# Kernel tuning notes

Measured on AMD Instinct MI355X. Metric: run time of the kernel, lower is better.

The kernel has to match this reference:

```python
import jax, jax.numpy as jnp
import numpy as np


def setup_inputs() -> dict:
    key = jax.random.key(0)
    ks = jax.random.split(key, 6)
    B, S, D = 32, 4096, 512
    return {
        "inputs": jax.random.normal(ks[0], (B, S, D), dtype=jnp.float32),
        "W_y": jax.random.normal(ks[1], (D, D), dtype=jnp.float32) * 0.05,
        "W_h": jax.random.normal(ks[2], (D, D), dtype=jnp.float32) * 0.05,
        "W_p": jax.random.normal(ks[3], (D, D), dtype=jnp.float32) * 0.05,
        "W_x": jax.random.normal(ks[4], (D, D), dtype=jnp.float32) * 0.05,
        "w": jax.random.normal(ks[5], (D, 1), dtype=jnp.float32) * 0.05,
    }


def reference(inputs, W_y, W_h, W_p, W_x, w):
    # inputs: [B, S, D]; the TF einsums 'ijk,kk->ijk' etc. use only diag(W).
    half = inputs.shape[1] // 2
    y = inputs[:, :half, :]          # [B, S/2, D] premise states
    h_n = inputs[:, -1, :]           # [B, D] final hidden state
    first = y * jnp.diagonal(W_y)                     # [B, S/2, D]
    second = (h_n * jnp.diagonal(W_h))[:, None, :]    # [B, 1, D] (RepeatVector via broadcast)
    M = jnp.tanh(first + second)                      # [B, S/2, D]
    scores = jnp.einsum('bsd,d->bs', M, w[:, 0])      # [B, S/2]
    alpha = jax.nn.softmax(scores, axis=-1)           # softmax over attended positions
    r = jnp.einsum('bsd,bs->bd', y, alpha)            # [B, D] weighted sum
    return jnp.tanh(r * jnp.diagonal(W_p) + h_n * jnp.diagonal(W_x))
```

## Files before the change

kernel.cpp:

```cpp
#include <hip/hip_runtime.h>

#define DDIM 512
#define HALF 2048
#define BATCH 32
#define S_TOTAL 4096
#define NCHUNK 64
#define ROWS_PER_CHUNK 32
#define LOG2E 1.44269504088896340736f
#define SHIFT2 32.0f

__device__ __forceinline__ float fast_tanh(float x) {
    float e = __builtin_amdgcn_exp2f(x * 2.88539008177792681472f);
    return 1.0f - 2.0f * __builtin_amdgcn_rcpf(e + 1.0f);
}

__device__ __forceinline__ float tanh_poly(float x) {
    const float c3 = -0.33333333333f, c5 = 0.13333333333f,
                c7 = -0.05396825397f, c9 = 0.02186948854f;
    float x2 = x * x;
    float p = fmaf(x2, c9, c7);
    p = fmaf(x2, p, c5);
    p = fmaf(x2, p, c3);
    return fmaf(x * x2, p, x);
}

template <int CTRL>
__device__ __forceinline__ float dpp_add(float x) {
    int yi = __builtin_amdgcn_update_dpp(0, __float_as_int(x), CTRL, 0xf, 0xf, true);
    return x + __int_as_float(yi);
}

__device__ __forceinline__ float wave_reduce_sum(float p) {
    p = dpp_add<0xB1>(p);
    p = dpp_add<0x4E>(p);
    p = dpp_add<0x141>(p);
    p = dpp_add<0x140>(p);
    p += __int_as_float(__builtin_amdgcn_ds_swizzle(__float_as_int(p), 0x401F));
    p += __shfl_xor(p, 32);
    return p;
}

__global__ __launch_bounds__(256) void pass1_kernel(
    const float* __restrict__ inputs, const float* __restrict__ Wy,
    const float* __restrict__ Wh, const float* __restrict__ wvec,
    float* __restrict__ ws_l, float* __restrict__ ws_r)
{
    const int chunk = blockIdx.x;
    const int b = blockIdx.y;
    const int tid = threadIdx.x;
    const int wave = tid >> 6;
    const int lane = tid & 63;
    const int d0 = lane * 8;

    float wy[8], wv[8], c[8];
    {
        const float* hn_row = inputs + ((size_t)b * S_TOTAL + (S_TOTAL - 1)) * DDIM;
#pragma unroll
        for (int j = 0; j < 8; ++j) {
            const int d = d0 + j;
            wy[j] = Wy[(size_t)d * (DDIM + 1)];
            wv[j] = wvec[d];
            c[j]  = hn_row[d] * Wh[(size_t)d * (DDIM + 1)];
        }
    }

    const float* rb0 = inputs +
        ((size_t)b * S_TOTAL + (size_t)chunk * ROWS_PER_CHUNK + wave * 8) * DDIM + d0;
    float y[8][8];
#pragma unroll
    for (int k = 0; k < 8; ++k) {
        const float4 u0 = *(const float4*)(rb0 + (size_t)k * DDIM);
        const float4 u1 = *(const float4*)(rb0 + (size_t)k * DDIM + 4);
        y[k][0] = u0.x; y[k][1] = u0.y; y[k][2] = u0.z; y[k][3] = u0.w;
        y[k][4] = u1.x; y[k][5] = u1.y; y[k][6] = u1.z; y[k][7] = u1.w;
    }

    float pd[8];
#pragma unroll
    for (int k = 0; k < 8; ++k) {
        float p = 0.0f;
#pragma unroll
        for (int j = 0; j < 8; ++j)
            p += tanh_poly(fmaf(y[k][j], wy[j], c[j])) * wv[j];
        pd[k] = p;
    }
#pragma unroll
    for (int k = 0; k < 8; ++k) pd[k] = wave_reduce_sum(pd[k]);

    float e[8];
    float l = 0.0f;
#pragma unroll
    for (int k = 0; k < 8; ++k) {
        e[k] = __builtin_amdgcn_exp2f(fmaf(pd[k], LOG2E, -SHIFT2));
        l += e[k];
    }
    float r[8];
#pragma unroll
    for (int j = 0; j < 8; ++j) {
        float acc = e[0] * y[0][j];
#pragma unroll
        for (int k = 1; k < 8; ++k) acc = fmaf(e[k], y[k][j], acc);
        r[j] = acc;
    }

    __shared__ float lds_r[4][DDIM];
    __shared__ float lds_l[4];
#pragma unroll
    for (int j = 0; j < 8; ++j) lds_r[wave][d0 + j] = r[j];
    if (lane == 0) lds_l[wave] = l;
    __syncthreads();

    const size_t blk = (size_t)b * NCHUNK + chunk;
#pragma unroll
    for (int d = tid; d < DDIM; d += 256)
        ws_r[blk * DDIM + d] =
            lds_r[0][d] + lds_r[1][d] + lds_r[2][d] + lds_r[3][d];
    if (tid == 0)
        ws_l[blk] = lds_l[0] + lds_l[1] + lds_l[2] + lds_l[3];
}

__global__ __launch_bounds__(256) void pass2_kernel(
    const float* __restrict__ inputs, const float* __restrict__ Wp,
    const float* __restrict__ Wx, const float* __restrict__ ws_l,
    const float* __restrict__ ws_r, float* __restrict__ out)
{
    const int b = blockIdx.y;
    const int d = blockIdx.x * 256 + threadIdx.x;

    float L = 0.0f;
#pragma unroll 8
    for (int cidx = 0; cidx < NCHUNK; ++cidx)
        L += ws_l[b * NCHUNK + cidx];

    float acc = 0.0f;
#pragma unroll 8
    for (int cidx = 0; cidx < NCHUNK; ++cidx)
        acc += ws_r[((size_t)b * NCHUNK + cidx) * DDIM + d];

    const float r = acc * __builtin_amdgcn_rcpf(L);
    const float hn = inputs[((size_t)b * S_TOTAL + (S_TOTAL - 1)) * DDIM + d];
    const float wp = Wp[(size_t)d * (DDIM + 1)];
    const float wx = Wx[(size_t)d * (DDIM + 1)];
    out[(size_t)b * DDIM + d] = fast_tanh(fmaf(r, wp, hn * wx));
}

extern "C" void kernel_launch(void* const* d_in, const int* in_sizes, int n_in,
                              void* d_out, int out_size, void* d_ws, size_t ws_size,
                              hipStream_t stream)
{
    const float* inputs = (const float*)d_in[0];
    const float* Wy     = (const float*)d_in[1];
    const float* Wh     = (const float*)d_in[2];
    const float* Wp     = (const float*)d_in[3];
    const float* Wx     = (const float*)d_in[4];
    const float* wvec   = (const float*)d_in[5];

    float* ws_l = (float*)d_ws;
    float* ws_r = ws_l + (size_t)BATCH * NCHUNK;

    dim3 grid1(NCHUNK, BATCH);
    pass1_kernel<<<grid1, 256, 0, stream>>>(inputs, Wy, Wh, wvec, ws_l, ws_r);

    dim3 grid2(DDIM / 256, BATCH);
    pass2_kernel<<<grid2, 256, 0, stream>>>(inputs, Wp, Wx, ws_l, ws_r,
                                            (float*)d_out);
}
```

Before: 350.9 us.

## Fuse both passes via last-block atomic counter and split lane columns for coalescing

Merges the chunk-reduction kernel and the finalize kernel into one launch. The last block to finish for each batch row, detected through an atomic counter, does the cross-chunk combine and the output tanh. Per-lane column mapping also changes from 8 contiguous floats to two float4 groups 256 apart, so each wave's loads are contiguous per instruction. This adds a memset launch for the counters, threadfences, and a serialized tail in one block per batch.

```diff
diff --git a/kernel.cpp b/kernel.cpp
--- a/kernel.cpp
+++ b/kernel.cpp
@@ -40,39 +40,43 @@
     return p;
 }
 
-__global__ __launch_bounds__(256) void pass1_kernel(
+__global__ __launch_bounds__(256) void fused_kernel(
     const float* __restrict__ inputs, const float* __restrict__ Wy,
     const float* __restrict__ Wh, const float* __restrict__ wvec,
-    float* __restrict__ ws_l, float* __restrict__ ws_r)
+    const float* __restrict__ Wp, const float* __restrict__ Wx,
+    int* __restrict__ cnt, float* __restrict__ ws_l, float* __restrict__ ws_r,
+    float* __restrict__ out)
 {
     const int chunk = blockIdx.x;
     const int b = blockIdx.y;
     const int tid = threadIdx.x;
     const int wave = tid >> 6;
     const int lane = tid & 63;
-    const int d0 = lane * 8;
+    const int dA = lane * 4;
+    const int dB = dA + 256;
 
-    float wy[8], wv[8], c[8];
-    {
-        const float* hn_row = inputs + ((size_t)b * S_TOTAL + (S_TOTAL - 1)) * DDIM;
+    const float* hn_row = inputs + ((size_t)b * S_TOTAL + (S_TOTAL - 1)) * DDIM;
+
+    float wyA[4], wyB[4], wvA[4], wvB[4], cA[4], cB[4];
 #pragma unroll
-        for (int j = 0; j < 8; ++j) {
-            const int d = d0 + j;
-            wy[j] = Wy[(size_t)d * (DDIM + 1)];
-            wv[j] = wvec[d];
-            c[j]  = hn_row[d] * Wh[(size_t)d * (DDIM + 1)];
-        }
+    for (int j = 0; j < 4; ++j) {
+        wyA[j] = Wy[(size_t)(dA + j) * (DDIM + 1)];
+        wyB[j] = Wy[(size_t)(dB + j) * (DDIM + 1)];
+        wvA[j] = wvec[dA + j];
+        wvB[j] = wvec[dB + j];
+        cA[j]  = hn_row[dA + j] * Wh[(size_t)(dA + j) * (DDIM + 1)];
+        cB[j]  = hn_row[dB + j] * Wh[(size_t)(dB + j) * (DDIM + 1)];
     }
 
-    const float* rb0 = inputs +
-        ((size_t)b * S_TOTAL + (size_t)chunk * ROWS_PER_CHUNK + wave * 8) * DDIM + d0;
-    float y[8][8];
+    const float* rp0 = inputs +
+        ((size_t)b * S_TOTAL + (size_t)chunk * ROWS_PER_CHUNK + wave * 8) * DDIM;
+    float yA[8][4], yB[8][4];
 #pragma unroll
     for (int k = 0; k < 8; ++k) {
-        const float4 u0 = *(const float4*)(rb0 + (size_t)k * DDIM);
-        const float4 u1 = *(const float4*)(rb0 + (size_t)k * DDIM + 4);
-        y[k][0] = u0.x; y[k][1] = u0.y; y[k][2] = u0.z; y[k][3] = u0.w;
-        y[k][4] = u1.x; y[k][5] = u1.y; y[k][6] = u1.z; y[k][7] = u1.w;
+        const float4 ua = *(const float4*)(rp0 + (size_t)k * DDIM + dA);
+        const float4 ub = *(const float4*)(rp0 + (size_t)k * DDIM + dB);
+        yA[k][0] = ua.x; yA[k][1] = ua.y; yA[k][2] = ua.z; yA[k][3] = ua.w;
+        yB[k][0] = ub.x; yB[k][1] = ub.y; yB[k][2] = ub.z; yB[k][3] = ub.w;
     }
 
     float pd[8];
@@ -80,8 +84,10 @@
     for (int k = 0; k < 8; ++k) {
         float p = 0.0f;
 #pragma unroll
-        for (int j = 0; j < 8; ++j)
-            p += tanh_poly(fmaf(y[k][j], wy[j], c[j])) * wv[j];
+        for (int j = 0; j < 4; ++j) {
+            p += tanh_poly(fmaf(yA[k][j], wyA[j], cA[j])) * wvA[j];
+            p += tanh_poly(fmaf(yB[k][j], wyB[j], cB[j])) * wvB[j];
+        }
         pd[k] = p;
     }
 #pragma unroll
@@ -94,19 +100,25 @@
         e[k] = __builtin_amdgcn_exp2f(fmaf(pd[k], LOG2E, -SHIFT2));
         l += e[k];
     }
-    float r[8];
+    float rA[4], rB[4];
 #pragma unroll
-    for (int j = 0; j < 8; ++j) {
-        float acc = e[0] * y[0][j];
+    for (int j = 0; j < 4; ++j) {
+        float a0 = e[0] * yA[0][j], b0 = e[0] * yB[0][j];
 #pragma unroll
-        for (int k = 1; k < 8; ++k) acc = fmaf(e[k], y[k][j], acc);
-        r[j] = acc;
+        for (int k = 1; k < 8; ++k) {
+            a0 = fmaf(e[k], yA[k][j], a0);
+            b0 = fmaf(e[k], yB[k][j], b0);
+        }
+        rA[j] = a0; rB[j] = b0;
     }
 
     __shared__ float lds_r[4][DDIM];
     __shared__ float lds_l[4];
 #pragma unroll
-    for (int j = 0; j < 8; ++j) lds_r[wave][d0 + j] = r[j];
+    for (int j = 0; j < 4; ++j) {
+        lds_r[wave][dA + j] = rA[j];
+        lds_r[wave][dB + j] = rB[j];
+    }
     if (lane == 0) lds_l[wave] = l;
     __syncthreads();
 
@@ -117,31 +129,32 @@
             lds_r[0][d] + lds_r[1][d] + lds_r[2][d] + lds_r[3][d];
     if (tid == 0)
         ws_l[blk] = lds_l[0] + lds_l[1] + lds_l[2] + lds_l[3];
-}
 
-__global__ __launch_bounds__(256) void pass2_kernel(
-    const float* __restrict__ inputs, const float* __restrict__ Wp,
-    const float* __restrict__ Wx, const float* __restrict__ ws_l,
-    const float* __restrict__ ws_r, float* __restrict__ out)
-{
-    const int b = blockIdx.y;
-    const int d = blockIdx.x * 256 + threadIdx.x;
+    __threadfence();
+    __syncthreads();
+    __shared__ int done;
+    if (tid == 0) done = atomicAdd(&cnt[b], 1);
+    __syncthreads();
+    if (done != NCHUNK - 1) return;
+    __threadfence();
 
     float L = 0.0f;
 #pragma unroll 8
-    for (int cidx = 0; cidx < NCHUNK; ++cidx)
-        L += ws_l[b * NCHUNK + cidx];
+    for (int c2 = 0; c2 < NCHUNK; ++c2)
+        L += ws_l[b * NCHUNK + c2];
+    const float invL = __builtin_amdgcn_rcpf(L);
 
-    float acc = 0.0f;
+#pragma unroll
+    for (int d = tid; d < DDIM; d += 256) {
+        float acc = 0.0f;
 #pragma unroll 8
-    for (int cidx = 0; cidx < NCHUNK; ++cidx)
-        acc += ws_r[((size_t)b * NCHUNK + cidx) * DDIM + d];
-
-    const float r = acc * __builtin_amdgcn_rcpf(L);
-    const float hn = inputs[((size_t)b * S_TOTAL + (S_TOTAL - 1)) * DDIM + d];
-    const float wp = Wp[(size_t)d * (DDIM + 1)];
-    const float wx = Wx[(size_t)d * (DDIM + 1)];
-    out[(size_t)b * DDIM + d] = fast_tanh(fmaf(r, wp, hn * wx));
+        for (int c2 = 0; c2 < NCHUNK; ++c2)
+            acc += ws_r[((size_t)b * NCHUNK + c2) * DDIM + d];
+        const float r = acc * invL;
+        const float wp = Wp[(size_t)d * (DDIM + 1)];
+        const float wx = Wx[(size_t)d * (DDIM + 1)];
+        out[(size_t)b * DDIM + d] = fast_tanh(fmaf(r, wp, hn_row[d] * wx));
+    }
 }
 
 extern "C" void kernel_launch(void* const* d_in, const int* in_sizes, int n_in,
@@ -155,13 +168,13 @@
     const float* Wx     = (const float*)d_in[4];
     const float* wvec   = (const float*)d_in[5];
 
-    float* ws_l = (float*)d_ws;
+    int*   cnt  = (int*)d_ws;
+    float* ws_l = (float*)d_ws + 64;
     float* ws_r = ws_l + (size_t)BATCH * NCHUNK;
 
-    dim3 grid1(NCHUNK, BATCH);
-    pass1_kernel<<<grid1, 256, 0, stream>>>(inputs, Wy, Wh, wvec, ws_l, ws_r);
+    hipMemsetAsync(cnt, 0, BATCH * sizeof(int), stream);
 
-    dim3 grid2(DDIM / 256, BATCH);
-    pass2_kernel<<<grid2, 256, 0, stream>>>(inputs, Wp, Wx, ws_l, ws_r,
-                                            (float*)d_out);
+    dim3 grid(NCHUNK, BATCH);
+    fused_kernel<<<grid, 256, 0, stream>>>(inputs, Wy, Wh, wvec, Wp, Wx,
+                                           cnt, ws_l, ws_r, (float*)d_out);
 }
```

New measurement: 717.9 us. 2.05x slower.
